# Performance work log

Measured on AMD Instinct MI355X. Metric: run time of the kernel, lower is better.

Reference implementation:

```python
import jax, jax.numpy as jnp
import numpy as np

EPS = 1e-8
N_CLASSES = 5  # n_way


def setup_inputs() -> dict:
    key = jax.random.key(0)
    k1, k2, k3 = jax.random.split(key, 3)
    N, M, T, V, C, D, topk = 256, 2, 300, 25, 3, 256, 64
    x = jax.random.normal(k1, (N, C, T, V, M), dtype=jnp.float32)
    x_T = jax.random.normal(k2, (N * M * T, D), dtype=jnp.float32)
    labels = jax.random.randint(k3, (N * M * T,), 0, N_CLASSES, dtype=jnp.int64 if jax.config.jax_enable_x64 else jnp.int32)
    return {"x": x, "x_T": x_T, "labels": labels, "N": N, "M": M, "T": T, "topk": topk}


def reference(x, x_T, labels, N, M, T, topk):
    # Per-class statistics via segment reductions (replaces the per-class python loop)
    ones = jnp.ones(labels.shape, dtype=x_T.dtype)
    counts = jax.ops.segment_sum(ones, labels, num_segments=N_CLASSES)          # [K]
    sums = jax.ops.segment_sum(x_T, labels, num_segments=N_CLASSES)            # [K, D]
    class_mean = sums / jnp.maximum(counts, 1.0)[:, None]                       # [K, D]
    overall_mean = x_T.mean(axis=0)                                             # [D]

    # Per-frame intra-class distance, per-class inter distance (detached in torch)
    intra = ((x_T - class_mean[labels]) ** 2).sum(axis=1)                       # [N*M*T]
    inter = jax.lax.stop_gradient(((class_mean - overall_mean) ** 2).sum(axis=1))  # [K]

    Sw = intra.sum()
    Sb = (counts * inter).sum()
    loss = Sw / (Sb + EPS)

    # Frame importance scores -> topk frames per sample (averaged over persons M)
    frame_scores = inter[labels] / (intra + EPS)                                # [N*M*T]
    VF = frame_scores.reshape(N, M, T).mean(axis=1)                             # [N, T]
    _, idx = jax.lax.top_k(VF, topk)                                            # [N, topk]
    idx = jnp.sort(idx, axis=1)

    # Gather the selected frames along the T axis of x: [N, C, T, V, M] -> [N, C, topk, V, M]
    x_select = jnp.take_along_axis(x, idx[:, None, :, None, None], axis=2)
    return loss, x_select
```

## Files before the change

kernel.cpp:

```cpp
#include <hip/hip_runtime.h>

#define NROWS   153600
#define D       256
#define D4      64
#define NCLS    5
#define NSAMP   256
#define TT      300
#define TOPK    64
#define VM      50
#define EPSF    1e-8f

#define WS_SUMS   0
#define WS_CNT    1280
#define WS_SQ     1285
#define WS_ZERO_N 1288
#define WS_CMEAN  1288
#define WS_INTER  2568
#define WS_FS     2576

__global__ __launch_bounds__(256) void zero_kernel(float* __restrict__ ws) {
    int i = blockIdx.x * 256 + threadIdx.x;
    if (i < WS_ZERO_N) ws[i] = 0.0f;
}

__global__ __launch_bounds__(256) void class_sums_kernel(const float4* __restrict__ xT4,
                                                         const int* __restrict__ labels,
                                                         float* __restrict__ sums,
                                                         float* __restrict__ counts,
                                                         float* __restrict__ sumsq) {
    __shared__ float buf[4][NCLS][D];
    __shared__ float sbuf[4][8];
    const int tid  = threadIdx.x;
    const int sub  = tid >> 6;
    const int lane = tid & 63;
    const int r0   = blockIdx.x * 128 + sub * 32;

    float acc[NCLS][4];
    #pragma unroll
    for (int c = 0; c < NCLS; ++c)
        #pragma unroll
        for (int k = 0; k < 4; ++k) acc[c][k] = 0.0f;
    float cnt[NCLS] = {0.f, 0.f, 0.f, 0.f, 0.f};
    float sq = 0.0f;

    #pragma unroll 1
    for (int jb = 0; jb < 32; jb += 8) {
        int l[8]; float4 v[8];
        #pragma unroll
        for (int k = 0; k < 8; ++k) {
            const int r = r0 + jb + k;
            l[k] = labels[r];
            v[k] = xT4[(size_t)r * D4 + lane];
        }
        #pragma unroll
        for (int k = 0; k < 8; ++k) {
            sq += v[k].x * v[k].x + v[k].y * v[k].y + v[k].z * v[k].z + v[k].w * v[k].w;
            #pragma unroll
            for (int c = 0; c < NCLS; ++c) {
                const bool m = (l[k] == c);
                acc[c][0] += m ? v[k].x : 0.0f;
                acc[c][1] += m ? v[k].y : 0.0f;
                acc[c][2] += m ? v[k].z : 0.0f;
                acc[c][3] += m ? v[k].w : 0.0f;
                cnt[c]    += m ? 1.0f : 0.0f;
            }
        }
    }

    #pragma unroll
    for (int o = 32; o > 0; o >>= 1) sq += __shfl_xor(sq, o, 64);

    #pragma unroll
    for (int c = 0; c < NCLS; ++c)
        *(float4*)&buf[sub][c][lane * 4] =
            make_float4(acc[c][0], acc[c][1], acc[c][2], acc[c][3]);
    if (lane == 0) {
        #pragma unroll
        for (int c = 0; c < NCLS; ++c) sbuf[sub][c] = cnt[c];
        sbuf[sub][5] = sq;
    }
    __syncthreads();

    #pragma unroll
    for (int c = 0; c < NCLS; ++c) {
        const float s = buf[0][c][tid] + buf[1][c][tid] + buf[2][c][tid] + buf[3][c][tid];
        atomicAdd(&sums[c * D + tid], s);
    }
    if (tid < 6) {
        const float s = sbuf[0][tid] + sbuf[1][tid] + sbuf[2][tid] + sbuf[3][tid];
        if (tid < 5) atomicAdd(&counts[tid], s);
        else         atomicAdd(sumsq, s);
    }
}

__global__ __launch_bounds__(256) void finalize_kernel(const float* __restrict__ sums,
                                                       const float* __restrict__ counts,
                                                       const float* __restrict__ sumsq,
                                                       float* __restrict__ cmean,
                                                       float* __restrict__ inter,
                                                       float* __restrict__ out) {
    __shared__ float r1[256], r2[256];
    const int d = threadIdx.x;
    float s[NCLS];
    float osum = 0.0f;
    #pragma unroll
    for (int c = 0; c < NCLS; ++c) { s[c] = sums[c * D + d]; osum += s[c]; }
    const float om = osum / (float)NROWS;

    float sb = 0.0f, swn = 0.0f;
    #pragma unroll
    for (int c = 0; c < NCLS; ++c) {
        const float cnt = counts[c];
        const float mm  = s[c] / fmaxf(cnt, 1.0f);
        cmean[c * D + d] = mm;
        const float diff = mm - om;
        r1[d] = diff * diff;
        r2[d] = mm * mm;
        __syncthreads();
        for (int off = 128; off > 0; off >>= 1) {
            if (d < off) { r1[d] += r1[d + off]; r2[d] += r2[d + off]; }
            __syncthreads();
        }
        if (d == 0) {
            inter[c] = r1[0];
            sb  += cnt * r1[0];
            swn += cnt * r2[0];
        }
        __syncthreads();
    }
    if (d == 0) {
        const float Sw = sumsq[0] - swn;
        out[0] = Sw / (sb + EPSF);
    }
}

__global__ __launch_bounds__(256) void intra_kernel(const float4* __restrict__ xT4,
                                                    const int* __restrict__ labels,
                                                    const float4* __restrict__ cmean4,
                                                    const float* __restrict__ inter,
                                                    float* __restrict__ fs) {
    __shared__ float cm[NCLS * D];
    __shared__ float sinter[NCLS];
    const int tid  = threadIdx.x;
    const int sub  = tid >> 6;
    const int lane = tid & 63;

    for (int i = tid; i < NCLS * D4; i += 256)
        ((float4*)cm)[i] = cmean4[i];
    if (tid < NCLS) sinter[tid] = inter[tid];
    __syncthreads();

    const int r0 = blockIdx.x * 128 + sub * 32;
    #pragma unroll 1
    for (int jb = 0; jb < 32; jb += 8) {
        int l[8]; float4 xv[8];
        #pragma unroll
        for (int k = 0; k < 8; ++k) {
            const int r = r0 + jb + k;
            l[k]  = labels[r];
            xv[k] = xT4[(size_t)r * D4 + lane];
        }
        float p[8];
        #pragma unroll
        for (int k = 0; k < 8; ++k) {
            const float4 mv = *(const float4*)&cm[l[k] * D + lane * 4];
            const float dx = xv[k].x - mv.x, dy = xv[k].y - mv.y;
            const float dz = xv[k].z - mv.z, dw = xv[k].w - mv.w;
            p[k] = dx * dx + dy * dy + dz * dz + dw * dw;
        }
        #pragma unroll
        for (int o = 32; o > 0; o >>= 1)
            #pragma unroll
            for (int k = 0; k < 8; ++k)
                p[k] += __shfl_xor(p[k], o, 64);
        if (lane == 0) {
            #pragma unroll
            for (int k = 0; k < 8; ++k)
                fs[r0 + jb + k] = sinter[l[k]] / (p[k] + EPSF);
        }
    }
}

__global__ __launch_bounds__(256) void topk_gather_kernel(const float* __restrict__ fs,
                                                          const float* __restrict__ x,
                                                          float* __restrict__ out) {
    __shared__ float VF[TT];
    __shared__ int   rnk[TT];
    __shared__ int   idxL[TOPK];
    const int n   = blockIdx.x;
    const int tid = threadIdx.x;

    const float* f0 = fs + (size_t)n * (2 * TT);
    for (int t = tid; t < TT; t += 256) VF[t] = 0.5f * (f0[t] + f0[t + TT]);
    __syncthreads();

    for (int t = tid; t < TT; t += 256) {
        const float v = VF[t];
        int r = 0;
        for (int u = 0; u < TT; ++u) {
            const float w = VF[u];
            r += (w > v) || (w == v && u < t);
        }
        rnk[t] = r;
    }
    __syncthreads();

    for (int t = tid; t < TT; t += 256) {
        if (rnk[t] < TOPK) {
            int pos = 0;
            for (int u = 0; u < t; ++u) pos += (rnk[u] < TOPK);
            idxL[pos] = t;
        }
    }
    __syncthreads();

    const float* xb = x + (size_t)n * 3 * TT * VM;
    float* ob = out + 1 + (size_t)n * 3 * TOPK * VM;
    for (int o = tid; o < 3 * TOPK * VM; o += 256) {
        const int c   = o / (TOPK * VM);
        const int rem = o - c * (TOPK * VM);
        const int j   = rem / VM;
        const int s   = rem - j * VM;
        const int t   = idxL[j];
        ob[(c * TOPK + j) * VM + s] = xb[(c * TT + t) * VM + s];
    }
}

extern "C" void kernel_launch(void* const* d_in, const int* in_sizes, int n_in,
                              void* d_out, int out_size, void* d_ws, size_t ws_size,
                              hipStream_t stream) {
    const float* x      = (const float*)d_in[0];
    const float* xT     = (const float*)d_in[1];
    const int*   labels = (const int*)d_in[2];
    float* out = (float*)d_out;
    float* ws  = (float*)d_ws;

    float* sums   = ws + WS_SUMS;
    float* counts = ws + WS_CNT;
    float* sumsq  = ws + WS_SQ;
    float* cmean  = ws + WS_CMEAN;
    float* inter  = ws + WS_INTER;
    float* fs     = ws + WS_FS;

    hipLaunchKernelGGL(zero_kernel, dim3((WS_ZERO_N + 255) / 256), dim3(256), 0, stream, ws);
    hipLaunchKernelGGL(class_sums_kernel, dim3(NROWS / 128), dim3(256), 0, stream,
                       (const float4*)xT, labels, sums, counts, sumsq);
    hipLaunchKernelGGL(finalize_kernel, dim3(1), dim3(256), 0, stream,
                       sums, counts, sumsq, cmean, inter, out);
    hipLaunchKernelGGL(intra_kernel, dim3(NROWS / 128), dim3(256), 0, stream,
                       (const float4*)xT, labels, (const float4*)cmean, inter, fs);
    hipLaunchKernelGGL(topk_gather_kernel, dim3(NSAMP), dim3(256), 0, stream,
                       fs, x, out);
}
```

Baseline: 327.6 us.

## Use wave-uniform label branching, transposed shuffle reduction, and split topk from gather

Class sums now branch on the wave-uniform label via readfirstlane instead of masking all five classes per row. The intra kernel keeps class means in registers and selects them by uniform label, replacing the LDS copy. It also reduces eight rows with a butterfly merge rather than eight independent full shuffle trees. Top-k selection and the frame gather are split into two kernels so the gather runs on 768 blocks instead of 256, at the cost of an extra launch and an index buffer in workspace.

New measurement: 342.1 us. 4.4% more time.

```diff
diff --git a/kernel.cpp b/kernel.cpp
--- a/kernel.cpp
+++ b/kernel.cpp
@@ -17,6 +17,7 @@
 #define WS_CMEAN  1288
 #define WS_INTER  2568
 #define WS_FS     2576
+#define WS_IDX    156176
 
 __global__ __launch_bounds__(256) void zero_kernel(float* __restrict__ ws) {
     int i = blockIdx.x * 256 + threadIdx.x;
@@ -54,15 +55,15 @@
         }
         #pragma unroll
         for (int k = 0; k < 8; ++k) {
-            sq += v[k].x * v[k].x + v[k].y * v[k].y + v[k].z * v[k].z + v[k].w * v[k].w;
-            #pragma unroll
-            for (int c = 0; c < NCLS; ++c) {
-                const bool m = (l[k] == c);
-                acc[c][0] += m ? v[k].x : 0.0f;
-                acc[c][1] += m ? v[k].y : 0.0f;
-                acc[c][2] += m ? v[k].z : 0.0f;
-                acc[c][3] += m ? v[k].w : 0.0f;
-                cnt[c]    += m ? 1.0f : 0.0f;
+            const float4 vv = v[k];
+            sq = fmaf(vv.x, vv.x, fmaf(vv.y, vv.y, fmaf(vv.z, vv.z, fmaf(vv.w, vv.w, sq))));
+            const int ls = __builtin_amdgcn_readfirstlane(l[k]);
+            switch (ls) {
+                case 0: acc[0][0]+=vv.x; acc[0][1]+=vv.y; acc[0][2]+=vv.z; acc[0][3]+=vv.w; cnt[0]+=1.f; break;
+                case 1: acc[1][0]+=vv.x; acc[1][1]+=vv.y; acc[1][2]+=vv.z; acc[1][3]+=vv.w; cnt[1]+=1.f; break;
+                case 2: acc[2][0]+=vv.x; acc[2][1]+=vv.y; acc[2][2]+=vv.z; acc[2][3]+=vv.w; cnt[2]+=1.f; break;
+                case 3: acc[3][0]+=vv.x; acc[3][1]+=vv.y; acc[3][2]+=vv.z; acc[3][3]+=vv.w; cnt[3]+=1.f; break;
+                default: acc[4][0]+=vv.x; acc[4][1]+=vv.y; acc[4][2]+=vv.z; acc[4][3]+=vv.w; cnt[4]+=1.f; break;
             }
         }
     }
@@ -134,20 +135,27 @@
     }
 }
 
+__device__ __forceinline__ float merge2(float a, float b, int m, int lane) {
+    const float t = __shfl_xor(a, m, 64);
+    const float u = __shfl_xor(b, m, 64);
+    return (lane & m) ? (b + u) : (a + t);
+}
+
 __global__ __launch_bounds__(256) void intra_kernel(const float4* __restrict__ xT4,
                                                     const int* __restrict__ labels,
                                                     const float4* __restrict__ cmean4,
                                                     const float* __restrict__ inter,
                                                     float* __restrict__ fs) {
-    __shared__ float cm[NCLS * D];
     __shared__ float sinter[NCLS];
     const int tid  = threadIdx.x;
     const int sub  = tid >> 6;
     const int lane = tid & 63;
-
-    for (int i = tid; i < NCLS * D4; i += 256)
-        ((float4*)cm)[i] = cmean4[i];
     if (tid < NCLS) sinter[tid] = inter[tid];
+    const float4 m0 = cmean4[0 * D4 + lane];
+    const float4 m1 = cmean4[1 * D4 + lane];
+    const float4 m2 = cmean4[2 * D4 + lane];
+    const float4 m3 = cmean4[3 * D4 + lane];
+    const float4 m4 = cmean4[4 * D4 + lane];
     __syncthreads();
 
     const int r0 = blockIdx.x * 128 + sub * 32;
@@ -163,30 +171,34 @@
         float p[8];
         #pragma unroll
         for (int k = 0; k < 8; ++k) {
-            const float4 mv = *(const float4*)&cm[l[k] * D + lane * 4];
+            const int ls = __builtin_amdgcn_readfirstlane(l[k]);
+            const float4 mv = (ls == 0) ? m0 : (ls == 1) ? m1 : (ls == 2) ? m2
+                            : (ls == 3) ? m3 : m4;
             const float dx = xv[k].x - mv.x, dy = xv[k].y - mv.y;
             const float dz = xv[k].z - mv.z, dw = xv[k].w - mv.w;
-            p[k] = dx * dx + dy * dy + dz * dz + dw * dw;
-        }
-        #pragma unroll
-        for (int o = 32; o > 0; o >>= 1)
-            #pragma unroll
-            for (int k = 0; k < 8; ++k)
-                p[k] += __shfl_xor(p[k], o, 64);
-        if (lane == 0) {
-            #pragma unroll
-            for (int k = 0; k < 8; ++k)
-                fs[r0 + jb + k] = sinter[l[k]] / (p[k] + EPSF);
-        }
-    }
-}
-
-__global__ __launch_bounds__(256) void topk_gather_kernel(const float* __restrict__ fs,
-                                                          const float* __restrict__ x,
-                                                          float* __restrict__ out) {
+            p[k] = fmaf(dx, dx, fmaf(dy, dy, fmaf(dz, dz, dw * dw)));
+        }
+        const float q0 = merge2(p[0], p[1], 1, lane);
+        const float q1 = merge2(p[2], p[3], 1, lane);
+        const float q2 = merge2(p[4], p[5], 1, lane);
+        const float q3 = merge2(p[6], p[7], 1, lane);
+        const float t0 = merge2(q0, q1, 2, lane);
+        const float t1 = merge2(q2, q3, 2, lane);
+        float s = merge2(t0, t1, 4, lane);
+        s += __shfl_xor(s, 8, 64);
+        s += __shfl_xor(s, 16, 64);
+        s += __shfl_xor(s, 32, 64);
+        if (lane < 8) {
+            const int rr = r0 + jb + lane;
+            fs[rr] = sinter[labels[rr]] / (s + EPSF);
+        }
+    }
+}
+
+__global__ __launch_bounds__(256) void topk_select_kernel(const float* __restrict__ fs,
+                                                          int* __restrict__ idx) {
     __shared__ float VF[TT];
     __shared__ int   rnk[TT];
-    __shared__ int   idxL[TOPK];
     const int n   = blockIdx.x;
     const int tid = threadIdx.x;
 
@@ -209,20 +221,28 @@
         if (rnk[t] < TOPK) {
             int pos = 0;
             for (int u = 0; u < t; ++u) pos += (rnk[u] < TOPK);
-            idxL[pos] = t;
-        }
-    }
-    __syncthreads();
-
-    const float* xb = x + (size_t)n * 3 * TT * VM;
-    float* ob = out + 1 + (size_t)n * 3 * TOPK * VM;
-    for (int o = tid; o < 3 * TOPK * VM; o += 256) {
-        const int c   = o / (TOPK * VM);
-        const int rem = o - c * (TOPK * VM);
-        const int j   = rem / VM;
-        const int s   = rem - j * VM;
-        const int t   = idxL[j];
-        ob[(c * TOPK + j) * VM + s] = xb[(c * TT + t) * VM + s];
+            idx[n * TOPK + pos] = t;
+        }
+    }
+}
+
+__global__ __launch_bounds__(256) void gather_kernel(const int* __restrict__ idx,
+                                                     const float* __restrict__ x,
+                                                     float* __restrict__ out) {
+    __shared__ int id[TOPK];
+    const int n = blockIdx.x / 3;
+    const int c = blockIdx.x % 3;
+    const int tid = threadIdx.x;
+    if (tid < TOPK) id[tid] = idx[n * TOPK + tid];
+    __syncthreads();
+
+    const float* xb = x + ((size_t)(n * 3 + c)) * TT * VM;
+    float* ob = out + 1 + ((size_t)(n * 3 + c)) * TOPK * VM;
+    #pragma unroll 1
+    for (int o = tid; o < TOPK * VM; o += 256) {
+        const int j = o / VM;
+        const int s = o - j * VM;
+        ob[o] = xb[id[j] * VM + s];
     }
 }
 
@@ -241,6 +261,7 @@
     float* cmean  = ws + WS_CMEAN;
     float* inter  = ws + WS_INTER;
     float* fs     = ws + WS_FS;
+    int*   idx    = (int*)(ws + WS_IDX);
 
     hipLaunchKernelGGL(zero_kernel, dim3((WS_ZERO_N + 255) / 256), dim3(256), 0, stream, ws);
     hipLaunchKernelGGL(class_sums_kernel, dim3(NROWS / 128), dim3(256), 0, stream,
@@ -249,6 +270,6 @@
                        sums, counts, sumsq, cmean, inter, out);
     hipLaunchKernelGGL(intra_kernel, dim3(NROWS / 128), dim3(256), 0, stream,
                        (const float4*)xT, labels, (const float4*)cmean, inter, fs);
-    hipLaunchKernelGGL(topk_gather_kernel, dim3(NSAMP), dim3(256), 0, stream,
-                       fs, x, out);
-}
+    hipLaunchKernelGGL(topk_select_kernel, dim3(NSAMP), dim3(256), 0, stream, fs, idx);
+    hipLaunchKernelGGL(gather_kernel, dim3(NSAMP * 3), dim3(256), 0, stream, idx, x, out);
+}
```
